# Performance work log

Measured on AMD Instinct MI355X. Metric: run time of the kernel, lower is better.

Reference implementation:

```python
import jax, jax.numpy as jnp
import numpy as np
from jax import lax

# ---- module hyperparameters (from init_kwargs) ----
B = 8          # number of point clouds in the batch
NP = 4096      # points per cloud
C_IN = 64      # input feature channels
RATIO = 0.25   # fps ratio -> M_PER = 1024 centroids per cloud
R = 0.2        # ball-query radius
K = 64         # max_num_neighbors (hardcoded in the torch forward)
BIG = 1e10     # sentinel distance for out-of-radius pairs


def _fps(p, m):
    """Farthest point sampling on one cloud p:[Np,3] -> m local indices.
    Deterministic start at index 0 (torch_geometric uses a random start)."""
    mind = jnp.sum((p - p[0]) ** 2, axis=-1)  # [Np] dist^2 to first pick

    def step(mind, _):
        nxt = jnp.argmax(mind)
        d = jnp.sum((p - p[nxt]) ** 2, axis=-1)
        return jnp.minimum(mind, d), nxt

    _, rest = lax.scan(step, mind, None, length=m - 1)
    return jnp.concatenate([jnp.zeros((1,), rest.dtype), rest])  # [m]


def _ball_knn(p, s):
    """Radius query with neighbor cap: for each sampled point, the K nearest
    points within radius R (same cloud). p:[Np,3], s:[m] -> idx [m,K], mask [m,K].
    Note: every centroid contains itself (d=0), so each row has >=1 valid entry."""
    q = p[s]                                              # [m,3]
    d2 = jnp.sum((q[:, None, :] - p[None, :, :]) ** 2, axis=-1)  # [m,Np]
    dm = jnp.where(d2 <= R * R, d2, BIG)
    negv, idx = lax.top_k(-dm, K)                         # nearest-K within ball
    return idx, (-negv) < (BIG * 0.5)


def setup_inputs() -> dict:
    key = jax.random.key(0)
    k = jax.random.split(key, 6)
    x = jax.random.normal(k[0], (B * NP, C_IN), dtype=jnp.float32)
    pos = jax.random.uniform(k[1], (B * NP, 3), dtype=jnp.float32)  # unit cube
    batch = jnp.repeat(jnp.arange(B, dtype=jnp.int32), NP)

    def lin(kk, fi, fo):
        return jax.random.normal(kk, (fi, fo), dtype=jnp.float32) / np.float32(np.sqrt(fi))

    W1 = lin(k[2], C_IN + 3, 64); b1 = jnp.zeros((64,), jnp.float32)
    W2 = lin(k[3], 64, 64);       b2 = jnp.zeros((64,), jnp.float32)
    W3 = lin(k[4], 64, 128);      b3 = jnp.zeros((128,), jnp.float32)
    return dict(x=x, pos=pos, batch=batch, W1=W1, b1=b1, W2=W2, b2=b2,
                W3=W3, b3=b3, num_graphs=B)


def reference(x, pos, batch, W1, b1, W2, b2, W3, b3, num_graphs):
    Bn = int(num_graphs)
    N = pos.shape[0]
    Np = N // Bn
    m = int(Np * RATIO)

    posb = pos.reshape(Bn, Np, 3)
    sel = jax.vmap(lambda p: _fps(p, m))(posb)          # [B,m] local idx
    nbr, mask = jax.vmap(_ball_knn)(posb, sel)          # [B,m,K]

    offs = jnp.arange(Bn, dtype=sel.dtype) * Np
    sel_g = (sel + offs[:, None]).reshape(-1)           # [M] global centroid idx
    nbr_g = (nbr + offs[:, None, None]).reshape(Bn * m, K)
    maskf = mask.reshape(Bn * m, K)

    pos_s = pos[sel_g]                                  # [M,3]
    rel = pos[nbr_g] - pos_s[:, None, :]                # [M,K,3] pos_j - pos_i
    h = jnp.concatenate([x[nbr_g], rel], axis=-1)       # [M,K,C_IN+3]
    # PointNetConv local_nn (Linear-ReLU-Linear-ReLU-Linear), max aggregation
    h = jax.nn.relu(h @ W1 + b1)
    h = jax.nn.relu(h @ W2 + b2)
    h = h @ W3 + b3                                     # [M,K,128]
    h = jnp.where(maskf[:, :, None], h, jnp.float32(-1e30))
    x_out = jnp.max(h, axis=1)                          # [M,128]

    return x_out, pos_s, batch[sel_g]
```

## Files before the change

kernel.cpp:

```cpp
#include <hip/hip_runtime.h>
#include <math.h>

#define NB   8
#define NPTS 4096
#define MPER 1024
#define MTOT (NB*MPER)
#define CIN  64
#define KNN  64
#define CAP  512
#define R2D  0.04000000000000001

typedef unsigned int u32;
typedef unsigned long long u64;
typedef float v2f __attribute__((ext_vector_type(2)));
using s16x8 = __attribute__((ext_vector_type(8))) short;
using f32x4 = __attribute__((ext_vector_type(4))) float;

__device__ __forceinline__ float d2f(float ax, float ay, float az,
                                     float bx, float by, float bz) {
    float dx = __fsub_rn(ax, bx);
    float dy = __fsub_rn(ay, by);
    float dz = __fsub_rn(az, bz);
    return __fadd_rn(__fadd_rn(__fmul_rn(dx, dx), __fmul_rn(dy, dy)),
                     __fmul_rn(dz, dz));
}

__device__ __forceinline__ v2f pk_add(v2f a, v2f b) {
    v2f d;
    asm("v_pk_add_f32 %0, %1, %2" : "=v"(d) : "v"(a), "v"(b));
    return d;
}
__device__ __forceinline__ v2f pk_mul(v2f a, v2f b) {
    v2f d;
    asm("v_pk_mul_f32 %0, %1, %2" : "=v"(d) : "v"(a), "v"(b));
    return d;
}

__device__ __forceinline__ unsigned short f2bf(float f) {
    u32 x = __float_as_uint(f);
    u32 r = (x + 0x7fffu + ((x >> 16) & 1u)) >> 16;
    return (unsigned short)r;
}
__device__ __forceinline__ u32 pk2(float a, float b) {
    return (u32)f2bf(a) | ((u32)f2bf(b) << 16);
}

__device__ __forceinline__ f32x4 mfma16(s16x8 a, s16x8 b, f32x4 c) {
    return __builtin_amdgcn_mfma_f32_16x16x32_bf16(a, b, c, 0, 0, 0);
}

__device__ __forceinline__ u64 wave_max_u64_dpp(u64 key)
{
#define DPPMAX(ctrl, rmask) do {                                                   \
        u32 lo_ = (u32)key;                                                        \
        u32 hi_ = (u32)(key >> 32);                                                \
        u32 plo = (u32)__builtin_amdgcn_update_dpp(                                \
            0, (int)lo_, ctrl, rmask, 0xf, false);                                 \
        u32 phi = (u32)__builtin_amdgcn_update_dpp(                                \
            0, (int)hi_, ctrl, rmask, 0xf, false);                                 \
        u64 pk = ((u64)phi << 32) | plo;                                           \
        if (pk > key) key = pk;                                                    \
    } while (0)
    DPPMAX(0x111, 0xf);
    DPPMAX(0x112, 0xf);
    DPPMAX(0x114, 0xf);
    DPPMAX(0x118, 0xf);
    DPPMAX(0x142, 0xa);
    DPPMAX(0x143, 0xc);
#undef DPPMAX
    return key;
}

__global__ __launch_bounds__(256) void fps_kernel(const float* __restrict__ pos,
                                                  int* __restrict__ sel)
{
    const int b    = blockIdx.x;
    const int t    = threadIdx.x;
    const int lane = t & 63;
    const int wv   = t >> 6;
    const float* pb = pos + (size_t)b * NPTS * 3;

    __shared__ float4 lp[NPTS];
    __shared__ u64 part[2][4];

    v2f px[8], py[8], pz[8], mind[8];
#pragma unroll
    for (int pr = 0; pr < 8; ++pr) {
        int j0 = (2 * pr + 0) * 256 + t;
        int j1 = (2 * pr + 1) * 256 + t;
        float x0 = pb[j0 * 3 + 0], y0 = pb[j0 * 3 + 1], z0 = pb[j0 * 3 + 2];
        float x1 = pb[j1 * 3 + 0], y1 = pb[j1 * 3 + 1], z1 = pb[j1 * 3 + 2];
        px[pr] = v2f{x0, x1}; py[pr] = v2f{y0, y1}; pz[pr] = v2f{z0, z1};
        mind[pr] = v2f{3.0e38f, 3.0e38f};
        lp[j0] = float4{x0, y0, z0, 0.f};
        lp[j1] = float4{x1, y1, z1, 0.f};
    }
    if (t == 0) sel[b * MPER + 0] = b * NPTS + 0;
    __syncthreads();

    float4 c0 = lp[0];
    float cx = c0.x, cy = c0.y, cz = c0.z;

    for (int it = 1; it < MPER; ++it) {
        const v2f ncx = v2f{-cx, -cx};
        const v2f ncy = v2f{-cy, -cy};
        const v2f ncz = v2f{-cz, -cz};

        float bv = -1.0f; int bi = 0;
#pragma unroll
        for (int pr = 0; pr < 8; ++pr) {
            v2f dx = pk_add(px[pr], ncx);
            v2f dy = pk_add(py[pr], ncy);
            v2f dz = pk_add(pz[pr], ncz);
            v2f s  = pk_add(pk_mul(dx, dx), pk_mul(dy, dy));
            v2f d2 = pk_add(s, pk_mul(dz, dz));
            float m0 = fminf(mind[pr].x, d2.x);
            float m1 = fminf(mind[pr].y, d2.y);
            mind[pr].x = m0; mind[pr].y = m1;
            if (m0 > bv) { bv = m0; bi = (2 * pr + 0) * 256 + t; }
            if (m1 > bv) { bv = m1; bi = (2 * pr + 1) * 256 + t; }
        }

        u64 key = ((u64)__float_as_uint(bv) << 32) | (u32)(~bi);
        key = wave_max_u64_dpp(key);

        const int p = it & 1;
        if (lane == 63) part[p][wv] = key;
        __syncthreads();

        u64 k0 = part[p][0];
        u64 k1 = part[p][1];
        u64 k2 = part[p][2];
        u64 k3 = part[p][3];
        u64 ka = k0 > k1 ? k0 : k1;
        u64 kb = k2 > k3 ? k2 : k3;
        u64 km = ka > kb ? ka : kb;
        int pick = (int)(~(u32)km);

        float4 cc = lp[pick];
        cx = cc.x; cy = cc.y; cz = cc.z;
        if (t == 0) sel[b * MPER + it] = b * NPTS + pick;
    }
}

__global__ __launch_bounds__(256) void ballq_kernel(
    const float* __restrict__ pos, const int* __restrict__ sel,
    int* __restrict__ nbr, int* __restrict__ cnt,
    float* __restrict__ out_pos, float* __restrict__ out_batch)
{
    __shared__ float cd[4][CAP];
    __shared__ int   ci[4][CAP];

    const int wv   = threadIdx.x >> 6;
    const int lane = threadIdx.x & 63;
    const int c    = blockIdx.x * 4 + wv;
    const int sg   = sel[c];
    const int b    = c >> 10;
    const int base = b * NPTS;
    const float* pb = pos + (size_t)base * 3;
    const float qx = pos[(size_t)sg * 3 + 0];
    const float qy = pos[(size_t)sg * 3 + 1];
    const float qz = pos[(size_t)sg * 3 + 2];

    int n = 0;
    for (int r0 = 0; r0 < NPTS; r0 += 64) {
        const int j = r0 + lane;
        float x = pb[j * 3 + 0], y = pb[j * 3 + 1], z = pb[j * 3 + 2];
        float d2 = d2f(x, y, z, qx, qy, qz);
        bool inside = ((double)d2 <= R2D);
        unsigned long long m = __ballot(inside);
        if (inside) {
            int myoff = n + __popcll(m & ((1ull << lane) - 1ull));
            if (myoff < CAP) { cd[wv][myoff] = d2; ci[wv][myoff] = j; }
        }
        n += __popcll(m);
    }
    n = min(n, CAP);
    __syncthreads();

    for (int i = lane; i < n; i += 64) {
        float d = cd[wv][i]; int id = ci[wv][i];
        int rank = 0;
        for (int j = 0; j < n; ++j) {
            float dj = cd[wv][j]; int ij = ci[wv][j];
            rank += (dj < d || (dj == d && ij < id)) ? 1 : 0;
        }
        if (rank < KNN) nbr[(size_t)c * KNN + rank] = base + id;
    }
    if (lane == 0) {
        cnt[c] = min(n, KNN);
        out_pos[c * 3 + 0] = qx;
        out_pos[c * 3 + 1] = qy;
        out_pos[c * 3 + 2] = qz;
        out_batch[c] = (float)b;
    }
}

#define W1T_U 6656
#define W2T_U 4608
#define W3T_U 9216
#define WTOT_U 20480

__global__ __launch_bounds__(256) void prep_weights(
    const float* __restrict__ W1, const float* __restrict__ W2,
    const float* __restrict__ W3, unsigned short* __restrict__ wsW)
{
    int i = blockIdx.x * 256 + threadIdx.x;
    if (i >= WTOT_U) return;
    float v;
    if (i < W1T_U) {
        int cr = i / 104, k = i - cr * 104;
        v = (k < 67) ? W1[k * 64 + cr] : 0.0f;
    } else if (i < W1T_U + W2T_U) {
        int j = i - W1T_U;
        int cr = j / 72, k = j - cr * 72;
        v = (k < 64) ? W2[k * 64 + cr] : 0.0f;
    } else {
        int j = i - (W1T_U + W2T_U);
        int cr = j / 72, k = j - cr * 72;
        v = (k < 64) ? W3[k * 128 + cr] : 0.0f;
    }
    wsW[i] = f2bf(v);
}

__global__ __launch_bounds__(256) void mlp_kernel(
    const float* __restrict__ x, const float* __restrict__ pos,
    const int* __restrict__ nbr, const int* __restrict__ cnt,
    const float* __restrict__ out_pos,
    const unsigned short* __restrict__ wsW,
    const float* __restrict__ b1, const float* __restrict__ b2,
    const float* __restrict__ b3,
    float* __restrict__ out_x)
{
    __shared__ __align__(16) unsigned short smA[6656];
    __shared__ __align__(16) unsigned short smW[WTOT_U];

    const int c = blockIdx.x;
    const int t = threadIdx.x;
    const int n = cnt[c];

    {
        const uint4* src = (const uint4*)wsW;
        uint4* dst = (uint4*)smW;
#pragma unroll
        for (int i = 0; i < 10; ++i) dst[t + 256 * i] = src[t + 256 * i];
    }

    {
        const int k = t >> 2, g = t & 3;
        const bool valid = k < n;
        const int nb = valid ? nbr[(size_t)c * KNN + k] : 0;
        const float* xr = x + (size_t)nb * CIN + g * 16;
        float4 f0, f1, f2, f3;
        if (valid) {
            f0 = *(const float4*)(xr + 0);
            f1 = *(const float4*)(xr + 4);
            f2 = *(const float4*)(xr + 8);
            f3 = *(const float4*)(xr + 12);
        } else {
            f0 = float4{0.f, 0.f, 0.f, 0.f};
            f1 = f0; f2 = f0; f3 = f0;
        }
        uint4 ua = { pk2(f0.x, f0.y), pk2(f0.z, f0.w), pk2(f1.x, f1.y), pk2(f1.z, f1.w) };
        uint4 ub = { pk2(f2.x, f2.y), pk2(f2.z, f2.w), pk2(f3.x, f3.y), pk2(f3.z, f3.w) };
        *(uint4*)&smA[k * 104 + g * 16 + 0] = ua;
        *(uint4*)&smA[k * 104 + g * 16 + 8] = ub;
        if (g == 0) {
            float r0 = 0.f, r1 = 0.f, r2 = 0.f;
            if (valid) {
                float q0 = out_pos[c * 3 + 0];
                float q1 = out_pos[c * 3 + 1];
                float q2 = out_pos[c * 3 + 2];
                r0 = __fsub_rn(pos[(size_t)nb * 3 + 0], q0);
                r1 = __fsub_rn(pos[(size_t)nb * 3 + 1], q1);
                r2 = __fsub_rn(pos[(size_t)nb * 3 + 2], q2);
            }
            uint4 uz = { 0u, 0u, 0u, 0u };
            uint4 ur = { pk2(r0, r1), (u32)f2bf(r2), 0u, 0u };
            *(uint4*)&smA[k * 104 + 64] = ur;
            *(uint4*)&smA[k * 104 + 72] = uz;
            *(uint4*)&smA[k * 104 + 80] = uz;
            *(uint4*)&smA[k * 104 + 88] = uz;
            *(uint4*)&smA[k * 104 + 96] = uz;
        }
    }
    __syncthreads();

    const int l  = t & 63;
    const int w  = t >> 6;
    const int lr = l & 15;
    const int kg = l >> 4;

    float bias1[4], bias2[4];
#pragma unroll
    for (int nt = 0; nt < 4; ++nt) {
        bias1[nt] = b1[nt * 16 + lr];
        bias2[nt] = b2[nt * 16 + lr];
    }

    const unsigned short* W1t = smW;
    const unsigned short* W2t = smW + W1T_U;
    const unsigned short* W3t = smW + W1T_U + W2T_U;
    unsigned short* H1 = smW;
    unsigned short* H2 = smA;

    f32x4 acc1[4];
#pragma unroll
    for (int nt = 0; nt < 4; ++nt) acc1[nt] = f32x4{0.f, 0.f, 0.f, 0.f};
    {
        const int ao = (w * 16 + lr) * 104 + kg * 8;
        const int bo = lr * 104 + kg * 8;
#pragma unroll
        for (int kc = 0; kc < 3; ++kc) {
            s16x8 af = *(const s16x8*)&smA[ao + kc * 32];
#pragma unroll
            for (int nt = 0; nt < 4; ++nt) {
                s16x8 bf = *(const s16x8*)&W1t[bo + nt * 1664 + kc * 32];
                acc1[nt] = mfma16(af, bf, acc1[nt]);
            }
        }
    }
    __syncthreads();
#pragma unroll
    for (int nt = 0; nt < 4; ++nt) {
        const int col = nt * 16 + lr;
#pragma unroll
        for (int r = 0; r < 4; ++r) {
            const int row = w * 16 + kg * 4 + r;
            float v = fmaxf(acc1[nt][r] + bias1[nt], 0.0f);
            H1[row * 72 + col] = f2bf(v);
        }
    }
    __syncthreads();

    f32x4 acc2[4];
#pragma unroll
    for (int nt = 0; nt < 4; ++nt) acc2[nt] = f32x4{0.f, 0.f, 0.f, 0.f};
    {
        const int ao = (w * 16 + lr) * 72 + kg * 8;
        const int bo = lr * 72 + kg * 8;
#pragma unroll
        for (int kc = 0; kc < 2; ++kc) {
            s16x8 af = *(const s16x8*)&H1[ao + kc * 32];
#pragma unroll
            for (int nt = 0; nt < 4; ++nt) {
                s16x8 bf = *(const s16x8*)&W2t[bo + nt * 1152 + kc * 32];
                acc2[nt] = mfma16(af, bf, acc2[nt]);
            }
        }
    }
#pragma unroll
    for (int nt = 0; nt < 4; ++nt) {
        const int col = nt * 16 + lr;
#pragma unroll
        for (int r = 0; r < 4; ++r) {
            const int row = w * 16 + kg * 4 + r;
            float v = fmaxf(acc2[nt][r] + bias2[nt], 0.0f);
            H2[row * 72 + col] = f2bf(v);
        }
    }
    __syncthreads();

    f32x4 acc3[8];
#pragma unroll
    for (int nt = 0; nt < 8; ++nt) acc3[nt] = f32x4{0.f, 0.f, 0.f, 0.f};
    {
        const int ao = (w * 16 + lr) * 72 + kg * 8;
        const int bo = lr * 72 + kg * 8;
#pragma unroll
        for (int kc = 0; kc < 2; ++kc) {
            s16x8 af = *(const s16x8*)&H2[ao + kc * 32];
#pragma unroll
            for (int nt = 0; nt < 8; ++nt) {
                s16x8 bf = *(const s16x8*)&W3t[bo + nt * 1152 + kc * 32];
                acc3[nt] = mfma16(af, bf, acc3[nt]);
            }
        }
    }

    float pm[8];
#pragma unroll
    for (int nt = 0; nt < 8; ++nt) pm[nt] = -1e30f;
#pragma unroll
    for (int r = 0; r < 4; ++r) {
        const int row = w * 16 + kg * 4 + r;
        if (row < n) {
#pragma unroll
            for (int nt = 0; nt < 8; ++nt) pm[nt] = fmaxf(pm[nt], acc3[nt][r]);
        }
    }
#pragma unroll
    for (int nt = 0; nt < 8; ++nt) {
        pm[nt] = fmaxf(pm[nt], __shfl_xor(pm[nt], 16));
        pm[nt] = fmaxf(pm[nt], __shfl_xor(pm[nt], 32));
    }
    __syncthreads();
    float* pbuf = (float*)smA;
    if (kg == 0) {
#pragma unroll
        for (int nt = 0; nt < 8; ++nt) pbuf[w * 128 + nt * 16 + lr] = pm[nt];
    }
    __syncthreads();
    if (t < 128) {
        float m = fmaxf(fmaxf(pbuf[t], pbuf[128 + t]),
                        fmaxf(pbuf[256 + t], pbuf[384 + t]));
        out_x[(size_t)c * 128 + t] = m + b3[t];
    }
}

extern "C" void kernel_launch(void* const* d_in, const int* in_sizes, int n_in,
                              void* d_out, int out_size, void* d_ws, size_t ws_size,
                              hipStream_t stream)
{
    const float* x   = (const float*)d_in[0];
    const float* pos = (const float*)d_in[1];
    const float* W1 = (const float*)d_in[3];
    const float* b1 = (const float*)d_in[4];
    const float* W2 = (const float*)d_in[5];
    const float* b2 = (const float*)d_in[6];
    const float* W3 = (const float*)d_in[7];
    const float* b3 = (const float*)d_in[8];

    float* out_x     = (float*)d_out;
    float* out_pos   = out_x + (size_t)MTOT * 128;
    float* out_batch = out_pos + (size_t)MTOT * 3;

    int* sel = (int*)d_ws;
    int* nbr = sel + MTOT;
    int* cnt = nbr + (size_t)MTOT * KNN;
    unsigned short* wsW = (unsigned short*)(cnt + MTOT);

    prep_weights<<<(WTOT_U + 255) / 256, 256, 0, stream>>>(W1, W2, W3, wsW);
    fps_kernel<<<NB, 256, 0, stream>>>(pos, sel);
    ballq_kernel<<<MTOT / 4, 256, 0, stream>>>(pos, sel, nbr, cnt, out_pos, out_batch);
    mlp_kernel<<<MTOT, 256, 0, stream>>>(x, pos, nbr, cnt, out_pos, wsW,
                                         b1, b2, b3, out_x);
}
```

Before: 740.4 us.

## Fuse FPS, ball query and MLP into a persistent kernel with progress-flag streaming

```diff
diff --git a/kernel.cpp b/kernel.cpp
--- a/kernel.cpp
+++ b/kernel.cpp
@@ -7,7 +7,7 @@
 #define MTOT (NB*MPER)
 #define CIN  64
 #define KNN  64
-#define CAP  512
+#define PUB  16
 #define R2D  0.04000000000000001
 
 typedef unsigned int u32;
@@ -71,131 +71,6 @@
     return key;
 }
 
-__global__ __launch_bounds__(256) void fps_kernel(const float* __restrict__ pos,
-                                                  int* __restrict__ sel)
-{
-    const int b    = blockIdx.x;
-    const int t    = threadIdx.x;
-    const int lane = t & 63;
-    const int wv   = t >> 6;
-    const float* pb = pos + (size_t)b * NPTS * 3;
-
-    __shared__ float4 lp[NPTS];
-    __shared__ u64 part[2][4];
-
-    v2f px[8], py[8], pz[8], mind[8];
-#pragma unroll
-    for (int pr = 0; pr < 8; ++pr) {
-        int j0 = (2 * pr + 0) * 256 + t;
-        int j1 = (2 * pr + 1) * 256 + t;
-        float x0 = pb[j0 * 3 + 0], y0 = pb[j0 * 3 + 1], z0 = pb[j0 * 3 + 2];
-        float x1 = pb[j1 * 3 + 0], y1 = pb[j1 * 3 + 1], z1 = pb[j1 * 3 + 2];
-        px[pr] = v2f{x0, x1}; py[pr] = v2f{y0, y1}; pz[pr] = v2f{z0, z1};
-        mind[pr] = v2f{3.0e38f, 3.0e38f};
-        lp[j0] = float4{x0, y0, z0, 0.f};
-        lp[j1] = float4{x1, y1, z1, 0.f};
-    }
-    if (t == 0) sel[b * MPER + 0] = b * NPTS + 0;
-    __syncthreads();
-
-    float4 c0 = lp[0];
-    float cx = c0.x, cy = c0.y, cz = c0.z;
-
-    for (int it = 1; it < MPER; ++it) {
-        const v2f ncx = v2f{-cx, -cx};
-        const v2f ncy = v2f{-cy, -cy};
-        const v2f ncz = v2f{-cz, -cz};
-
-        float bv = -1.0f; int bi = 0;
-#pragma unroll
-        for (int pr = 0; pr < 8; ++pr) {
-            v2f dx = pk_add(px[pr], ncx);
-            v2f dy = pk_add(py[pr], ncy);
-            v2f dz = pk_add(pz[pr], ncz);
-            v2f s  = pk_add(pk_mul(dx, dx), pk_mul(dy, dy));
-            v2f d2 = pk_add(s, pk_mul(dz, dz));
-            float m0 = fminf(mind[pr].x, d2.x);
-            float m1 = fminf(mind[pr].y, d2.y);
-            mind[pr].x = m0; mind[pr].y = m1;
-            if (m0 > bv) { bv = m0; bi = (2 * pr + 0) * 256 + t; }
-            if (m1 > bv) { bv = m1; bi = (2 * pr + 1) * 256 + t; }
-        }
-
-        u64 key = ((u64)__float_as_uint(bv) << 32) | (u32)(~bi);
-        key = wave_max_u64_dpp(key);
-
-        const int p = it & 1;
-        if (lane == 63) part[p][wv] = key;
-        __syncthreads();
-
-        u64 k0 = part[p][0];
-        u64 k1 = part[p][1];
-        u64 k2 = part[p][2];
-        u64 k3 = part[p][3];
-        u64 ka = k0 > k1 ? k0 : k1;
-        u64 kb = k2 > k3 ? k2 : k3;
-        u64 km = ka > kb ? ka : kb;
-        int pick = (int)(~(u32)km);
-
-        float4 cc = lp[pick];
-        cx = cc.x; cy = cc.y; cz = cc.z;
-        if (t == 0) sel[b * MPER + it] = b * NPTS + pick;
-    }
-}
-
-__global__ __launch_bounds__(256) void ballq_kernel(
-    const float* __restrict__ pos, const int* __restrict__ sel,
-    int* __restrict__ nbr, int* __restrict__ cnt,
-    float* __restrict__ out_pos, float* __restrict__ out_batch)
-{
-    __shared__ float cd[4][CAP];
-    __shared__ int   ci[4][CAP];
-
-    const int wv   = threadIdx.x >> 6;
-    const int lane = threadIdx.x & 63;
-    const int c    = blockIdx.x * 4 + wv;
-    const int sg   = sel[c];
-    const int b    = c >> 10;
-    const int base = b * NPTS;
-    const float* pb = pos + (size_t)base * 3;
-    const float qx = pos[(size_t)sg * 3 + 0];
-    const float qy = pos[(size_t)sg * 3 + 1];
-    const float qz = pos[(size_t)sg * 3 + 2];
-
-    int n = 0;
-    for (int r0 = 0; r0 < NPTS; r0 += 64) {
-        const int j = r0 + lane;
-        float x = pb[j * 3 + 0], y = pb[j * 3 + 1], z = pb[j * 3 + 2];
-        float d2 = d2f(x, y, z, qx, qy, qz);
-        bool inside = ((double)d2 <= R2D);
-        unsigned long long m = __ballot(inside);
-        if (inside) {
-            int myoff = n + __popcll(m & ((1ull << lane) - 1ull));
-            if (myoff < CAP) { cd[wv][myoff] = d2; ci[wv][myoff] = j; }
-        }
-        n += __popcll(m);
-    }
-    n = min(n, CAP);
-    __syncthreads();
-
-    for (int i = lane; i < n; i += 64) {
-        float d = cd[wv][i]; int id = ci[wv][i];
-        int rank = 0;
-        for (int j = 0; j < n; ++j) {
-            float dj = cd[wv][j]; int ij = ci[wv][j];
-            rank += (dj < d || (dj == d && ij < id)) ? 1 : 0;
-        }
-        if (rank < KNN) nbr[(size_t)c * KNN + rank] = base + id;
-    }
-    if (lane == 0) {
-        cnt[c] = min(n, KNN);
-        out_pos[c * 3 + 0] = qx;
-        out_pos[c * 3 + 1] = qy;
-        out_pos[c * 3 + 2] = qz;
-        out_batch[c] = (float)b;
-    }
-}
-
 #define W1T_U 6656
 #define W2T_U 4608
 #define W3T_U 9216
@@ -223,189 +98,367 @@
     wsW[i] = f2bf(v);
 }
 
-__global__ __launch_bounds__(256) void mlp_kernel(
-    const float* __restrict__ x, const float* __restrict__ pos,
-    const int* __restrict__ nbr, const int* __restrict__ cnt,
-    const float* __restrict__ out_pos,
+__global__ __launch_bounds__(64) void init_sync(int* __restrict__ prog,
+                                                int* __restrict__ wq)
+{
+    int t = threadIdx.x;
+    if (t < NB) prog[t * 16] = -1;
+    if (t == NB) *wq = 0;
+}
+
+
+__device__ __forceinline__ void fps_body(char* smem, const float* __restrict__ pos,
+                                         int* __restrict__ sel, int* __restrict__ prog)
+{
+    const int b    = blockIdx.x;
+    const int t    = threadIdx.x;
+    const int lane = t & 63;
+    const int wv   = t >> 6;
+    const float* pb = pos + (size_t)b * NPTS * 3;
+
+    float4* lp = (float4*)smem;
+    u64*    part = (u64*)(smem + 65536);
+
+    v2f px[8], py[8], pz[8], mind[8];
+#pragma unroll
+    for (int pr = 0; pr < 8; ++pr) {
+        int j0 = (2 * pr + 0) * 256 + t;
+        int j1 = (2 * pr + 1) * 256 + t;
+        float x0 = pb[j0 * 3 + 0], y0 = pb[j0 * 3 + 1], z0 = pb[j0 * 3 + 2];
+        float x1 = pb[j1 * 3 + 0], y1 = pb[j1 * 3 + 1], z1 = pb[j1 * 3 + 2];
+        px[pr] = v2f{x0, x1}; py[pr] = v2f{y0, y1}; pz[pr] = v2f{z0, z1};
+        mind[pr] = v2f{3.0e38f, 3.0e38f};
+        lp[j0] = float4{x0, y0, z0, 0.f};
+        lp[j1] = float4{x1, y1, z1, 0.f};
+    }
+    if (t == 0)
+        __hip_atomic_store(&sel[b * MPER + 0], b * NPTS + 0,
+                           __ATOMIC_RELAXED, __HIP_MEMORY_SCOPE_AGENT);
+    __syncthreads();
+
+    float4 c0 = lp[0];
+    float cx = c0.x, cy = c0.y, cz = c0.z;
+
+    for (int it = 1; it < MPER; ++it) {
+        const v2f ncx = v2f{-cx, -cx};
+        const v2f ncy = v2f{-cy, -cy};
+        const v2f ncz = v2f{-cz, -cz};
+
+        float bv = -1.0f; int bi = 0;
+#pragma unroll
+        for (int pr = 0; pr < 8; ++pr) {
+            v2f dx = pk_add(px[pr], ncx);
+            v2f dy = pk_add(py[pr], ncy);
+            v2f dz = pk_add(pz[pr], ncz);
+            v2f s  = pk_add(pk_mul(dx, dx), pk_mul(dy, dy));
+            v2f d2 = pk_add(s, pk_mul(dz, dz));
+            float m0 = fminf(mind[pr].x, d2.x);
+            float m1 = fminf(mind[pr].y, d2.y);
+            mind[pr].x = m0; mind[pr].y = m1;
+            if (m0 > bv) { bv = m0; bi = (2 * pr + 0) * 256 + t; }
+            if (m1 > bv) { bv = m1; bi = (2 * pr + 1) * 256 + t; }
+        }
+
+        u64 key = ((u64)__float_as_uint(bv) << 32) | (u32)(~bi);
+        key = wave_max_u64_dpp(key);
+
+        const int p = it & 1;
+        if (lane == 63) part[p * 4 + wv] = key;
+        __syncthreads();
+
+        u64 k0 = part[p * 4 + 0];
+        u64 k1 = part[p * 4 + 1];
+        u64 k2 = part[p * 4 + 2];
+        u64 k3 = part[p * 4 + 3];
+        u64 ka = k0 > k1 ? k0 : k1;
+        u64 kb = k2 > k3 ? k2 : k3;
+        u64 km = ka > kb ? ka : kb;
+        int pick = (int)(~(u32)km);
+
+        float4 cc = lp[pick];
+        cx = cc.x; cy = cc.y; cz = cc.z;
+        if (t == 0) {
+            __hip_atomic_store(&sel[b * MPER + it], b * NPTS + pick,
+                               __ATOMIC_RELAXED, __HIP_MEMORY_SCOPE_AGENT);
+            if ((it & (PUB - 1)) == (PUB - 1))
+                __hip_atomic_store(&prog[b * 16], it,
+                                   __ATOMIC_RELEASE, __HIP_MEMORY_SCOPE_AGENT);
+        }
+    }
+}
+
+__device__ __forceinline__ void worker_loop(
+    char* smem, const float* __restrict__ pos, const float* __restrict__ x,
     const unsigned short* __restrict__ wsW,
     const float* __restrict__ b1, const float* __restrict__ b2,
     const float* __restrict__ b3,
-    float* __restrict__ out_x)
-{
-    __shared__ __align__(16) unsigned short smA[6656];
-    __shared__ __align__(16) unsigned short smW[WTOT_U];
-
-    const int c = blockIdx.x;
+    int* __restrict__ sel, int* __restrict__ prog, int* __restrict__ wq,
+    float* __restrict__ out_x, float* __restrict__ out_pos,
+    float* __restrict__ out_batch)
+{
     const int t = threadIdx.x;
-    const int n = cnt[c];
+    const int l = t & 63, w = t >> 6, lr = l & 15, kg = l >> 4;
+
+    unsigned short* sW   = (unsigned short*)smem;
+    unsigned short* sA1  = (unsigned short*)(smem + 40960);
+    unsigned short* sH1  = (unsigned short*)(smem + 54272);
+    unsigned short* sH2  = (unsigned short*)(smem + 63488);
+    float* cd   = (float*)(smem + 72704);
+    int*   ci   = (int*)(smem + 74752);
+    int*   nbrl = (int*)(smem + 76800);
+    int*   scnt = (int*)(smem + 77056);
+    float* sq   = (float*)(smem + 77072);
+    int*   sslot= (int*)(smem + 77084);
 
     {
         const uint4* src = (const uint4*)wsW;
-        uint4* dst = (uint4*)smW;
+        uint4* dst = (uint4*)sW;
 #pragma unroll
         for (int i = 0; i < 10; ++i) dst[t + 256 * i] = src[t + 256 * i];
     }
-
-    {
-        const int k = t >> 2, g = t & 3;
-        const bool valid = k < n;
-        const int nb = valid ? nbr[(size_t)c * KNN + k] : 0;
-        const float* xr = x + (size_t)nb * CIN + g * 16;
-        float4 f0, f1, f2, f3;
-        if (valid) {
-            f0 = *(const float4*)(xr + 0);
-            f1 = *(const float4*)(xr + 4);
-            f2 = *(const float4*)(xr + 8);
-            f3 = *(const float4*)(xr + 12);
-        } else {
-            f0 = float4{0.f, 0.f, 0.f, 0.f};
-            f1 = f0; f2 = f0; f3 = f0;
-        }
-        uint4 ua = { pk2(f0.x, f0.y), pk2(f0.z, f0.w), pk2(f1.x, f1.y), pk2(f1.z, f1.w) };
-        uint4 ub = { pk2(f2.x, f2.y), pk2(f2.z, f2.w), pk2(f3.x, f3.y), pk2(f3.z, f3.w) };
-        *(uint4*)&smA[k * 104 + g * 16 + 0] = ua;
-        *(uint4*)&smA[k * 104 + g * 16 + 8] = ub;
-        if (g == 0) {
-            float r0 = 0.f, r1 = 0.f, r2 = 0.f;
-            if (valid) {
-                float q0 = out_pos[c * 3 + 0];
-                float q1 = out_pos[c * 3 + 1];
-                float q2 = out_pos[c * 3 + 2];
-                r0 = __fsub_rn(pos[(size_t)nb * 3 + 0], q0);
-                r1 = __fsub_rn(pos[(size_t)nb * 3 + 1], q1);
-                r2 = __fsub_rn(pos[(size_t)nb * 3 + 2], q2);
-            }
-            uint4 uz = { 0u, 0u, 0u, 0u };
-            uint4 ur = { pk2(r0, r1), (u32)f2bf(r2), 0u, 0u };
-            *(uint4*)&smA[k * 104 + 64] = ur;
-            *(uint4*)&smA[k * 104 + 72] = uz;
-            *(uint4*)&smA[k * 104 + 80] = uz;
-            *(uint4*)&smA[k * 104 + 88] = uz;
-            *(uint4*)&smA[k * 104 + 96] = uz;
-        }
-    }
-    __syncthreads();
-
-    const int l  = t & 63;
-    const int w  = t >> 6;
-    const int lr = l & 15;
-    const int kg = l >> 4;
-
     float bias1[4], bias2[4];
 #pragma unroll
     for (int nt = 0; nt < 4; ++nt) {
         bias1[nt] = b1[nt * 16 + lr];
         bias2[nt] = b2[nt * 16 + lr];
     }
-
-    const unsigned short* W1t = smW;
-    const unsigned short* W2t = smW + W1T_U;
-    const unsigned short* W3t = smW + W1T_U + W2T_U;
-    unsigned short* H1 = smW;
-    unsigned short* H2 = smA;
-
-    f32x4 acc1[4];
-#pragma unroll
-    for (int nt = 0; nt < 4; ++nt) acc1[nt] = f32x4{0.f, 0.f, 0.f, 0.f};
-    {
-        const int ao = (w * 16 + lr) * 104 + kg * 8;
-        const int bo = lr * 104 + kg * 8;
-#pragma unroll
-        for (int kc = 0; kc < 3; ++kc) {
-            s16x8 af = *(const s16x8*)&smA[ao + kc * 32];
-#pragma unroll
-            for (int nt = 0; nt < 4; ++nt) {
-                s16x8 bf = *(const s16x8*)&W1t[bo + nt * 1664 + kc * 32];
-                acc1[nt] = mfma16(af, bf, acc1[nt]);
-            }
-        }
-    }
-    __syncthreads();
-#pragma unroll
-    for (int nt = 0; nt < 4; ++nt) {
-        const int col = nt * 16 + lr;
+    const float b3r = (t < 128) ? b3[t] : 0.0f;
+
+    const unsigned short* W1t = sW;
+    const unsigned short* W2t = sW + W1T_U;
+    const unsigned short* W3t = sW + W1T_U + W2T_U;
+
+    for (;;) {
+        if (t == 0) {
+            int s = __hip_atomic_fetch_add(wq, 1, __ATOMIC_RELAXED,
+                                           __HIP_MEMORY_SCOPE_AGENT);
+            sslot[0] = s;
+            if (s < MTOT) {
+                const int it = s >> 3, b = s & 7;
+                const int c = b * MPER + it;
+                int p_;
+                do {
+                    p_ = __hip_atomic_load(&prog[b * 16], __ATOMIC_ACQUIRE,
+                                           __HIP_MEMORY_SCOPE_AGENT);
+                    if (p_ < it) __builtin_amdgcn_s_sleep(32);
+                } while (p_ < it);
+                int sg = __hip_atomic_load(&sel[c], __ATOMIC_RELAXED,
+                                           __HIP_MEMORY_SCOPE_AGENT);
+                float qx = pos[(size_t)sg * 3 + 0];
+                float qy = pos[(size_t)sg * 3 + 1];
+                float qz = pos[(size_t)sg * 3 + 2];
+                sq[0] = qx; sq[1] = qy; sq[2] = qz;
+                out_pos[(size_t)c * 3 + 0] = qx;
+                out_pos[(size_t)c * 3 + 1] = qy;
+                out_pos[(size_t)c * 3 + 2] = qz;
+                out_batch[c] = (float)b;
+            }
+        }
+        __syncthreads();
+        const int s = sslot[0];
+        if (s >= MTOT) break;
+        const int it = s >> 3, b = s & 7;
+        const int c = b * MPER + it;
+        const float qx = sq[0], qy = sq[1], qz = sq[2];
+
+        const float* pb2 = pos + (size_t)b * NPTS * 3;
+        int nw = 0;
+        for (int r0 = 0; r0 < 1024; r0 += 64) {
+            int j = w * 1024 + r0 + l;
+            float xx = pb2[j * 3 + 0], yy = pb2[j * 3 + 1], zz = pb2[j * 3 + 2];
+            float d2 = d2f(xx, yy, zz, qx, qy, qz);
+            bool inside = ((double)d2 <= R2D);
+            u64 m = __ballot(inside);
+            if (inside) {
+                int off = nw + __popcll(m & ((1ull << l) - 1ull));
+                if (off < 128) { cd[w * 128 + off] = d2; ci[w * 128 + off] = j; }
+            }
+            nw += __popcll(m);
+        }
+        nw = min(nw, 128);
+        if (l == 0) scnt[w] = nw;
+        __syncthreads();
+        const int n0 = scnt[0], n1 = scnt[1], n2 = scnt[2], n3 = scnt[3];
+        const int ntot = n0 + n1 + n2 + n3;
+        const int cnt = min(ntot, KNN);
+
+        for (int f = t; f < ntot; f += 256) {
+            int w2, i2;
+            if (f < n0)                { w2 = 0; i2 = f; }
+            else if (f < n0 + n1)      { w2 = 1; i2 = f - n0; }
+            else if (f < n0 + n1 + n2) { w2 = 2; i2 = f - n0 - n1; }
+            else                       { w2 = 3; i2 = f - n0 - n1 - n2; }
+            float d = cd[w2 * 128 + i2]; int id = ci[w2 * 128 + i2];
+            int rank = 0;
+#pragma unroll
+            for (int w3 = 0; w3 < 4; ++w3) {
+                int nn = scnt[w3];
+                for (int j = 0; j < nn; ++j) {
+                    float dj = cd[w3 * 128 + j]; int ij = ci[w3 * 128 + j];
+                    rank += (dj < d || (dj == d && ij < id)) ? 1 : 0;
+                }
+            }
+            if (rank < KNN) nbrl[rank] = id;
+        }
+        __syncthreads();
+
+        {
+            const int k = t >> 2, g = t & 3;
+            const bool valid = k < cnt;
+            const int nbg = valid ? (b * NPTS + nbrl[k]) : 0;
+            const float* xr = x + (size_t)nbg * CIN + g * 16;
+            float4 f0, f1, f2, f3;
+            if (valid) {
+                f0 = *(const float4*)(xr + 0);
+                f1 = *(const float4*)(xr + 4);
+                f2 = *(const float4*)(xr + 8);
+                f3 = *(const float4*)(xr + 12);
+            } else {
+                f0 = float4{0.f, 0.f, 0.f, 0.f};
+                f1 = f0; f2 = f0; f3 = f0;
+            }
+            uint4 ua = { pk2(f0.x, f0.y), pk2(f0.z, f0.w), pk2(f1.x, f1.y), pk2(f1.z, f1.w) };
+            uint4 ub = { pk2(f2.x, f2.y), pk2(f2.z, f2.w), pk2(f3.x, f3.y), pk2(f3.z, f3.w) };
+            *(uint4*)&sA1[k * 104 + g * 16 + 0] = ua;
+            *(uint4*)&sA1[k * 104 + g * 16 + 8] = ub;
+            if (g == 0) {
+                float r0 = 0.f, r1 = 0.f, r2 = 0.f;
+                if (valid) {
+                    r0 = __fsub_rn(pos[(size_t)nbg * 3 + 0], qx);
+                    r1 = __fsub_rn(pos[(size_t)nbg * 3 + 1], qy);
+                    r2 = __fsub_rn(pos[(size_t)nbg * 3 + 2], qz);
+                }
+                uint4 uz = { 0u, 0u, 0u, 0u };
+                uint4 ur = { pk2(r0, r1), (u32)f2bf(r2), 0u, 0u };
+                *(uint4*)&sA1[k * 104 + 64] = ur;
+                *(uint4*)&sA1[k * 104 + 72] = uz;
+                *(uint4*)&sA1[k * 104 + 80] = uz;
+                *(uint4*)&sA1[k * 104 + 88] = uz;
+                *(uint4*)&sA1[k * 104 + 96] = uz;
+            }
+        }
+        __syncthreads();
+
+        f32x4 acc1[4];
+#pragma unroll
+        for (int nt = 0; nt < 4; ++nt) acc1[nt] = f32x4{0.f, 0.f, 0.f, 0.f};
+        {
+            const int ao = (w * 16 + lr) * 104 + kg * 8;
+            const int bo = lr * 104 + kg * 8;
+#pragma unroll
+            for (int kc = 0; kc < 3; ++kc) {
+                s16x8 af = *(const s16x8*)&sA1[ao + kc * 32];
+#pragma unroll
+                for (int nt = 0; nt < 4; ++nt) {
+                    s16x8 bf = *(const s16x8*)&W1t[bo + nt * 1664 + kc * 32];
+                    acc1[nt] = mfma16(af, bf, acc1[nt]);
+                }
+            }
+        }
+#pragma unroll
+        for (int nt = 0; nt < 4; ++nt) {
+            const int col = nt * 16 + lr;
+#pragma unroll
+            for (int r = 0; r < 4; ++r) {
+                const int row = w * 16 + kg * 4 + r;
+                float v = fmaxf(acc1[nt][r] + bias1[nt], 0.0f);
+                sH1[row * 72 + col] = f2bf(v);
+            }
+        }
+        __syncthreads();
+
+        f32x4 acc2[4];
+#pragma unroll
+        for (int nt = 0; nt < 4; ++nt) acc2[nt] = f32x4{0.f, 0.f, 0.f, 0.f};
+        {
+            const int ao = (w * 16 + lr) * 72 + kg * 8;
+            const int bo = lr * 72 + kg * 8;
+#pragma unroll
+            for (int kc = 0; kc < 2; ++kc) {
+                s16x8 af = *(const s16x8*)&sH1[ao + kc * 32];
+#pragma unroll
+                for (int nt = 0; nt < 4; ++nt) {
+                    s16x8 bf = *(const s16x8*)&W2t[bo + nt * 1152 + kc * 32];
+                    acc2[nt] = mfma16(af, bf, acc2[nt]);
+                }
+            }
+        }
+#pragma unroll
+        for (int nt = 0; nt < 4; ++nt) {
+            const int col = nt * 16 + lr;
+#pragma unroll
+            for (int r = 0; r < 4; ++r) {
+                const int row = w * 16 + kg * 4 + r;
+                float v = fmaxf(acc2[nt][r] + bias2[nt], 0.0f);
+                sH2[row * 72 + col] = f2bf(v);
+            }
+        }
+        __syncthreads();
+
+        f32x4 acc3[8];
+#pragma unroll
+        for (int nt = 0; nt < 8; ++nt) acc3[nt] = f32x4{0.f, 0.f, 0.f, 0.f};
+        {
+            const int ao = (w * 16 + lr) * 72 + kg * 8;
+            const int bo = lr * 72 + kg * 8;
+#pragma unroll
+            for (int kc = 0; kc < 2; ++kc) {
+                s16x8 af = *(const s16x8*)&sH2[ao + kc * 32];
+#pragma unroll
+                for (int nt = 0; nt < 8; ++nt) {
+                    s16x8 bf = *(const s16x8*)&W3t[bo + nt * 1152 + kc * 32];
+                    acc3[nt] = mfma16(af, bf, acc3[nt]);
+                }
+            }
+        }
+
+        float pm[8];
+#pragma unroll
+        for (int nt = 0; nt < 8; ++nt) pm[nt] = -1e30f;
 #pragma unroll
         for (int r = 0; r < 4; ++r) {
             const int row = w * 16 + kg * 4 + r;
-            float v = fmaxf(acc1[nt][r] + bias1[nt], 0.0f);
-            H1[row * 72 + col] = f2bf(v);
-        }
-    }
-    __syncthreads();
-
-    f32x4 acc2[4];
-#pragma unroll
-    for (int nt = 0; nt < 4; ++nt) acc2[nt] = f32x4{0.f, 0.f, 0.f, 0.f};
-    {
-        const int ao = (w * 16 + lr) * 72 + kg * 8;
-        const int bo = lr * 72 + kg * 8;
-#pragma unroll
-        for (int kc = 0; kc < 2; ++kc) {
-            s16x8 af = *(const s16x8*)&H1[ao + kc * 32];
-#pragma unroll
-            for (int nt = 0; nt < 4; ++nt) {
-                s16x8 bf = *(const s16x8*)&W2t[bo + nt * 1152 + kc * 32];
-                acc2[nt] = mfma16(af, bf, acc2[nt]);
-            }
-        }
-    }
-#pragma unroll
-    for (int nt = 0; nt < 4; ++nt) {
-        const int col = nt * 16 + lr;
-#pragma unroll
-        for (int r = 0; r < 4; ++r) {
-            const int row = w * 16 + kg * 4 + r;
-            float v = fmaxf(acc2[nt][r] + bias2[nt], 0.0f);
-            H2[row * 72 + col] = f2bf(v);
-        }
-    }
-    __syncthreads();
-
-    f32x4 acc3[8];
-#pragma unroll
-    for (int nt = 0; nt < 8; ++nt) acc3[nt] = f32x4{0.f, 0.f, 0.f, 0.f};
-    {
-        const int ao = (w * 16 + lr) * 72 + kg * 8;
-        const int bo = lr * 72 + kg * 8;
-#pragma unroll
-        for (int kc = 0; kc < 2; ++kc) {
-            s16x8 af = *(const s16x8*)&H2[ao + kc * 32];
-#pragma unroll
-            for (int nt = 0; nt < 8; ++nt) {
-                s16x8 bf = *(const s16x8*)&W3t[bo + nt * 1152 + kc * 32];
-                acc3[nt] = mfma16(af, bf, acc3[nt]);
-            }
-        }
-    }
-
-    float pm[8];
-#pragma unroll
-    for (int nt = 0; nt < 8; ++nt) pm[nt] = -1e30f;
-#pragma unroll
-    for (int r = 0; r < 4; ++r) {
-        const int row = w * 16 + kg * 4 + r;
-        if (row < n) {
-#pragma unroll
-            for (int nt = 0; nt < 8; ++nt) pm[nt] = fmaxf(pm[nt], acc3[nt][r]);
-        }
-    }
-#pragma unroll
-    for (int nt = 0; nt < 8; ++nt) {
-        pm[nt] = fmaxf(pm[nt], __shfl_xor(pm[nt], 16));
-        pm[nt] = fmaxf(pm[nt], __shfl_xor(pm[nt], 32));
-    }
-    __syncthreads();
-    float* pbuf = (float*)smA;
-    if (kg == 0) {
-#pragma unroll
-        for (int nt = 0; nt < 8; ++nt) pbuf[w * 128 + nt * 16 + lr] = pm[nt];
-    }
-    __syncthreads();
-    if (t < 128) {
-        float m = fmaxf(fmaxf(pbuf[t], pbuf[128 + t]),
-                        fmaxf(pbuf[256 + t], pbuf[384 + t]));
-        out_x[(size_t)c * 128 + t] = m + b3[t];
-    }
+            if (row < cnt) {
+#pragma unroll
+                for (int nt = 0; nt < 8; ++nt) pm[nt] = fmaxf(pm[nt], acc3[nt][r]);
+            }
+        }
+#pragma unroll
+        for (int nt = 0; nt < 8; ++nt) {
+            pm[nt] = fmaxf(pm[nt], __shfl_xor(pm[nt], 16));
+            pm[nt] = fmaxf(pm[nt], __shfl_xor(pm[nt], 32));
+        }
+        __syncthreads();
+        float* pbuf = cd;
+        if (kg == 0) {
+#pragma unroll
+            for (int nt = 0; nt < 8; ++nt) pbuf[w * 128 + nt * 16 + lr] = pm[nt];
+        }
+        __syncthreads();
+        if (t < 128) {
+            float m = fmaxf(fmaxf(pbuf[t], pbuf[128 + t]),
+                            fmaxf(pbuf[256 + t], pbuf[384 + t]));
+            out_x[(size_t)c * 128 + t] = m + b3r;
+        }
+    }
+}
+
+__global__ __launch_bounds__(256) void fused_kernel(
+    const float* __restrict__ pos, const float* __restrict__ x,
+    const unsigned short* __restrict__ wsW,
+    const float* __restrict__ b1, const float* __restrict__ b2,
+    const float* __restrict__ b3,
+    int* __restrict__ sel, int* __restrict__ prog, int* __restrict__ wq,
+    float* __restrict__ out_x, float* __restrict__ out_pos,
+    float* __restrict__ out_batch)
+{
+    extern __shared__ char smem[];
+    if (blockIdx.x < NB) {
+        fps_body(smem, pos, sel, prog);
+        __syncthreads();
+    }
+    worker_loop(smem, pos, x, wsW, b1, b2, b3, sel, prog, wq,
+                out_x, out_pos, out_batch);
 }
 
 extern "C" void kernel_launch(void* const* d_in, const int* in_sizes, int n_in,
@@ -425,14 +478,17 @@
     float* out_pos   = out_x + (size_t)MTOT * 128;
     float* out_batch = out_pos + (size_t)MTOT * 3;
 
-    int* sel = (int*)d_ws;
-    int* nbr = sel + MTOT;
-    int* cnt = nbr + (size_t)MTOT * KNN;
-    unsigned short* wsW = (unsigned short*)(cnt + MTOT);
+    int* sel  = (int*)d_ws;
+    int* prog = sel + MTOT;
+    int* wq   = prog + 128;
+    unsigned short* wsW = (unsigned short*)(wq + 16);
+
+    (void)hipFuncSetAttribute((const void*)fused_kernel,
+                              hipFuncAttributeMaxDynamicSharedMemorySize, 86016);
 
     prep_weights<<<(WTOT_U + 255) / 256, 256, 0, stream>>>(W1, W2, W3, wsW);
-    fps_kernel<<<NB, 256, 0, stream>>>(pos, sel);
-    ballq_kernel<<<MTOT / 4, 256, 0, stream>>>(pos, sel, nbr, cnt, out_pos, out_batch);
-    mlp_kernel<<<MTOT, 256, 0, stream>>>(x, pos, nbr, cnt, out_pos, wsW,
-                                         b1, b2, b3, out_x);
-}
+    init_sync<<<1, 64, 0, stream>>>(prog, wq);
+    fused_kernel<<<256, 256, 86016, stream>>>(pos, x, wsW, b1, b2, b3,
+                                              sel, prog, wq,
+                                              out_x, out_pos, out_batch);
+}
```

Result: faster. 713.3 us (-3.7%).
